# Kernel tuning notes

Hardware: AMD Instinct MI355X
Metric: run time of the kernel (lower is better)

Reference implementation:

```python
import jax, jax.numpy as jnp
import numpy as np
from jax import lax

N = 100000          # nodes in the AST
D = 128             # embedding_dims
C = 8               # max arity (complete 8-ary tree)
NTYPES = 131        # len(NODE_TYPES)


def setup_inputs() -> dict:
    key = jax.random.key(0)
    k_t, k_e, k_ih, k_hh = jax.random.split(key, 4)

    # --- build complete 8-ary tree structure (numpy, static) ---
    idx = np.arange(1, N)
    par = (idx - 1) // C
    slot = (idx - 1) % C
    children = np.full((N, C), N, dtype=np.int32)   # pad with sentinel N
    children[par, slot] = idx
    num_children = np.bincount(par, minlength=N).astype(np.int32)
    # depth of node i in complete C-ary tree: level d starts at (C^d-1)/(C-1)
    starts = np.array([(C ** d - 1) // (C - 1) for d in range(12)], dtype=np.int64)
    depth = np.searchsorted(starts, np.arange(N), side='right') - 1
    L = int(depth.max()) + 1
    M = int(np.bincount(depth).max())
    level_nodes = np.full((L, M), N, dtype=np.int32)  # deepest level first
    for d in range(L):
        nd = np.nonzero(depth == d)[0].astype(np.int32)
        level_nodes[L - 1 - d, : len(nd)] = nd

    # --- parameters (xavier-ish embedding, small LSTM weights, torch bias init) ---
    emb_table = jax.random.normal(k_e, (NTYPES, D), jnp.float32) * (2.0 / (NTYPES + D)) ** 0.5
    W_ih = jax.random.normal(k_ih, (4 * D, D), jnp.float32) * (2.0 / (5 * D)) ** 0.5
    W_hh = jax.random.normal(k_hh, (4 * D, D), jnp.float32) * (2.0 / (5 * D)) ** 0.5
    b_ih = jnp.zeros((4 * D,), jnp.float32)
    b_hh = jnp.ones((4 * D,), jnp.float32)
    node_types = jax.random.randint(k_t, (N,), 0, NTYPES, dtype=jnp.int32)
    return {
        'emb_table': emb_table, 'W_ih': W_ih, 'W_hh': W_hh,
        'b_ih': b_ih, 'b_hh': b_hh,
        'node_types': node_types,
        'children': jnp.asarray(children),
        'num_children': jnp.asarray(num_children),
        'level_nodes': jnp.asarray(level_nodes),
    }


def _forward(emb_table, W_ih, W_hh, b_ih, b_hh, node_types, children, num_children, level_nodes):
    M = level_nodes.shape[1]
    T = C + 1  # sequence length = parent emb + up to C child results

    def level_step(results, nodes):
        # nodes: [M] node ids for this depth level (sentinel N = padding)
        emb = emb_table[node_types[nodes]]            # [M, D] (OOB gather clips; masked below)
        nc = num_children[nodes]                      # [M]
        cres = results[children[nodes]]               # [M, C, D]; sentinel -> zero row N
        seq = jnp.concatenate([emb[:, None, :], cres], axis=1)  # [M, T, D]

        def cell(carry, xt):
            h, c = carry
            x, t = xt
            gates = x @ W_ih.T + b_ih + h @ W_hh.T + b_hh      # [M, 4D]
            i, f, g, o = jnp.split(gates, 4, axis=-1)
            i = jax.nn.sigmoid(i); f = jax.nn.sigmoid(f)
            g = jnp.tanh(g); o = jax.nn.sigmoid(o)
            c_new = f * c + i * g
            h_new = o * jnp.tanh(c_new)
            valid = (t <= nc)[:, None]                         # steps 0..nc are real
            return (jnp.where(valid, h_new, h), jnp.where(valid, c_new, c)), None

        h0 = jnp.zeros((M, emb_table.shape[1]), emb_table.dtype)
        (h, _), _ = lax.scan(cell, (h0, h0), (seq.transpose(1, 0, 2), jnp.arange(T)))
        out = jnp.where((nc == 0)[:, None], emb, h)   # leaves: raw embedding, no LSTM
        results = results.at[nodes].set(out)
        results = results.at[N].set(0.0)              # keep sentinel row zero
        return results, None

    results0 = jnp.zeros((N + 1, emb_table.shape[1]), emb_table.dtype)
    results, _ = lax.scan(level_step, results0, level_nodes)  # deepest -> root
    return results[0]  # root (Module node) encoding, shape [D]


def reference(emb_table, W_ih, W_hh, b_ih, b_hh, node_types, children, num_children, level_nodes):
    return _forward(emb_table, W_ih, W_hh, b_ih, b_hh,
                    node_types, children, num_children, level_nodes)
```

## Files before the change

### kernel.cpp

```cpp
#include <hip/hip_runtime.h>


#define D 128
#define NTOT 100000
#define NINT 12500
#define NTYPES 131

typedef _Float16 f16x8 __attribute__((ext_vector_type(8)));
typedef _Float16 f16x4 __attribute__((ext_vector_type(4)));
typedef float    f32x4 __attribute__((ext_vector_type(4)));

__device__ __forceinline__ float fsig(float x) {
    return __builtin_amdgcn_rcpf(1.f + __expf(-x));
}
__device__ __forceinline__ float ftanh(float x) {
    return 1.f - 2.f * __builtin_amdgcn_rcpf(__expf(2.f * x) + 1.f);
}

template<int DPT> struct XVT;
template<> struct XVT<8> { using T = f16x8; };
template<> struct XVT<4> { using T = f16x4; };

__global__ void prep(const float* __restrict__ W_ih, const float* __restrict__ W_hh,
                     const float* __restrict__ b_ih, const float* __restrict__ b_hh,
                     const float* __restrict__ emb,
                     _Float16* __restrict__ wfrag, float4* __restrict__ bias4,
                     _Float16* __restrict__ embH)
{
    int t = blockIdx.x * blockDim.x + threadIdx.x;
    if (t < 8 * 4 * 8 * 64) {
        int l  = t & 63;
        int kk = (t >> 6) & 7;
        int ct = (t >> 9) & 3;
        int w  = (t >> 11) & 7;
        int k0 = (kk & 3) * 32 + ((l >> 4) * 8);
        int c  = ct * 128 + w * 16 + (l & 15);
        const float* src = (kk < 4) ? (W_ih + (size_t)c * D + k0)
                                    : (W_hh + (size_t)c * D + k0);
        f16x8 v;
#pragma unroll
        for (int j = 0; j < 8; ++j) v[j] = (_Float16)src[j];
        *(f16x8*)(wfrag + (size_t)t * 8) = v;
    }
    if (t < D) {
        bias4[t] = make_float4(b_ih[t      ] + b_hh[t      ],
                               b_ih[t + 128] + b_hh[t + 128],
                               b_ih[t + 256] + b_hh[t + 256],
                               b_ih[t + 384] + b_hh[t + 384]);
    }
    if (t < NTYPES * D / 8) {
        f16x8 v;
#pragma unroll
        for (int j = 0; j < 8; ++j) v[j] = (_Float16)emb[t * 8 + j];
        *(f16x8*)(embH + (size_t)t * 8) = v;
    }
}

template<int RT, bool FUSE_ROOT>
__global__ __launch_bounds__(512) void lstm_level(
    int start, int count,
    const _Float16* __restrict__ embH, const int* __restrict__ node_types,
    const int* __restrict__ children,
    const _Float16* __restrict__ wfrag, const float4* __restrict__ bias4,
    _Float16* __restrict__ resultsH, float* __restrict__ out)
{
    constexpr int NR  = 16 * RT;
    constexpr int TPR = 512 / NR;
    constexpr int DPT = 128 / TPR;
    using xvec = typename XVT<DPT>::T;

    __shared__ __align__(16) _Float16 Xh[2][NR][264];
    __shared__ int chid_s[NR][8];
    __shared__ int chty_s[NR][8];
    __shared__ __align__(16) _Float16 Hstash[8][128];

    const int t  = threadIdx.x;
    const int w  = t >> 6;
    const int l  = t & 63;
    const int n0 = start + (int)blockIdx.x * NR;
    const int B  = min(NR, start + count - n0);

    const int row  = t / TPR;
    const int di   = (t % TPR) * DPT;
    const int dcol = w * 16 + (l & 15);

    if (t < NR * 8) {
        int rr = t >> 3, slot = t & 7;
        int ch = children[(size_t)(n0 + rr) * 8 + slot];
        chid_s[rr][slot] = ch;
        chty_s[rr][slot] = (ch >= NINT && ch < NTOT) ? node_types[ch] : 0;
    }

    f16x8 bf[4][8];
#pragma unroll
    for (int ct = 0; ct < 4; ++ct)
#pragma unroll
        for (int kk = 0; kk < 8; ++kk)
            bf[ct][kk] = *(const f16x8*)(wfrag + ((size_t)(((w * 4 + ct) * 8 + kk) * 64 + l)) * 8);
    const float4 bb = bias4[dcol];

    __syncthreads();

    auto issue_gather = [&](int s) -> xvec {
        const _Float16* src;
        if (s == 0) {
            src = embH + (size_t)node_types[n0 + row] * D + di;
        } else {
            int ch = chid_s[row][s - 1];
            if (ch >= NTOT) return (xvec)(_Float16)0.f;
            src = (ch < NINT) ? (resultsH + (size_t)ch * D + di)
                              : (embH + (size_t)chty_s[row][s - 1] * D + di);
        }
        return *(const xvec*)src;
    };

    *(xvec*)&Xh[0][row][di]       = issue_gather(0);
    *(xvec*)&Xh[0][row][128 + di] = (xvec)(_Float16)0.f;
    xvec xA = issue_gather(1);
    xvec xB = issue_gather(2);

    float cr[RT][4], hr[RT][4];
#pragma unroll
    for (int rt = 0; rt < RT; ++rt)
#pragma unroll
        for (int r = 0; r < 4; ++r) { cr[rt][r] = 0.f; hr[rt][r] = 0.f; }

    f32x4 acc[RT][4];
    auto mfma_phase = [&](int b) {
#pragma unroll
        for (int rt = 0; rt < RT; ++rt)
#pragma unroll
            for (int ct = 0; ct < 4; ++ct) acc[rt][ct] = (f32x4){0.f, 0.f, 0.f, 0.f};
#pragma unroll
        for (int kk = 0; kk < 8; ++kk) {
#pragma unroll
            for (int rt = 0; rt < RT; ++rt) {
                f16x8 a = *(const f16x8*)&Xh[b][rt * 16 + (l & 15)][kk * 32 + ((l >> 4) * 8)];
#pragma unroll
                for (int ct = 0; ct < 4; ++ct)
                    acc[rt][ct] = __builtin_amdgcn_mfma_f32_16x16x32_f16(a, bf[ct][kk], acc[rt][ct], 0, 0, 0);
            }
        }
    };
    auto cell_phase = [&](int s, int b, bool always) {
#pragma unroll
        for (int rt = 0; rt < RT; ++rt)
#pragma unroll
            for (int r = 0; r < 4; ++r) {
                const int r2 = rt * 16 + ((l >> 4) * 4) + r;
                const bool upd = always || (s == 0) || (chid_s[r2][s - 1] < NTOT);
                if (upd) {
                    float iv = fsig (acc[rt][0][r] + bb.x);
                    float fv = fsig (acc[rt][1][r] + bb.y);
                    float gv = ftanh(acc[rt][2][r] + bb.z);
                    float ov = fsig (acc[rt][3][r] + bb.w);
                    float cn = fv * cr[rt][r] + iv * gv;
                    cr[rt][r] = cn;
                    hr[rt][r] = ov * ftanh(cn);
                }
                if (s < 8) Xh[b ^ 1][r2][128 + dcol] = (_Float16)hr[rt][r];
            }
    };

    __syncthreads();

    for (int s = 0; s < 9; ++s) {
        const int b = s & 1;
        mfma_phase(b);
        if (s < 8) {
            *(xvec*)&Xh[b ^ 1][row][di] = xA;
            xA = xB;
            if (s <= 5) xB = issue_gather(s + 3);
        }
        cell_phase(s, b, false);
        __syncthreads();
    }

#pragma unroll
    for (int rt = 0; rt < RT; ++rt)
#pragma unroll
        for (int r = 0; r < 4; ++r) {
            const int r2 = rt * 16 + ((l >> 4) * 4) + r;
            if (r2 < B) {
                resultsH[(size_t)(n0 + r2) * D + dcol] = (_Float16)hr[rt][r];
                if (FUSE_ROOT && r2 < 8) Hstash[r2][dcol] = (_Float16)hr[rt][r];
            }
        }

    if constexpr (FUSE_ROOT) {
        __syncthreads();
        *(xvec*)&Xh[0][row][di]       = *(const xvec*)(embH + (size_t)node_types[0] * D + di);
        *(xvec*)&Xh[0][row][128 + di] = (xvec)(_Float16)0.f;
#pragma unroll
        for (int rt = 0; rt < RT; ++rt)
#pragma unroll
            for (int r = 0; r < 4; ++r) { cr[rt][r] = 0.f; hr[rt][r] = 0.f; }
        __syncthreads();

        for (int s = 0; s < 9; ++s) {
            const int b = s & 1;
            mfma_phase(b);
            if (s < 8)
                *(xvec*)&Xh[b ^ 1][row][di] = *(const xvec*)&Hstash[s][di];
            cell_phase(s, b, true);
            __syncthreads();
        }
        if ((l >> 4) == 0) out[dcol] = hr[0][0];
    }
}

extern "C" void kernel_launch(void* const* d_in, const int* in_sizes, int n_in,
                              void* d_out, int out_size, void* d_ws, size_t ws_size,
                              hipStream_t stream)
{
    const float* emb        = (const float*)d_in[0];
    const float* W_ih       = (const float*)d_in[1];
    const float* W_hh       = (const float*)d_in[2];
    const float* b_ih       = (const float*)d_in[3];
    const float* b_hh       = (const float*)d_in[4];
    const int*   node_types = (const int*)d_in[5];
    const int*   children   = (const int*)d_in[6];

    float* out = (float*)d_out;

    char*      ws       = (char*)d_ws;
    _Float16*  resultsH = (_Float16*)ws;
    size_t     off      = ((size_t)NINT * D * 2 + 255) & ~(size_t)255;
    _Float16*  wfrag    = (_Float16*)(ws + off);
    float4*    bias4    = (float4*)(ws + off + 262144);
    _Float16*  embH     = (_Float16*)(ws + off + 262144 + 2048);

    prep<<<66, 256, 0, stream>>>(W_ih, W_hh, b_ih, b_hh, emb, wfrag, bias4, embH);

    lstm_level<2,false><<<245, 512, 0, stream>>>(4681, 7819, embH, node_types, children,
                                                 wfrag, bias4, resultsH, out);
    lstm_level<1,false><<<256, 512, 0, stream>>>(585, 4096, embH, node_types, children,
                                                 wfrag, bias4, resultsH, out);
    lstm_level<1,false><<<32, 512, 0, stream>>>(73, 512, embH, node_types, children,
                                                wfrag, bias4, resultsH, out);
    lstm_level<1,false><<<4, 512, 0, stream>>>(9, 64, embH, node_types, children,
                                               wfrag, bias4, resultsH, out);
    lstm_level<1,true><<<1, 512, 0, stream>>>(1, 8, embH, node_types, children,
                                              wfrag, bias4, resultsH, out);
}
```

Measured before the change: 106.2 us.

## Fuse prep and all tree levels into one persistent kernel with grid barriers

Replaces the prep kernel and the five per-level launches with a single persistent kernel of 256 blocks that synchronise through atomic-counter grid barriers in global memory. Every level now uses 32-row tiles, so level 2 runs on 128 blocks instead of 256 and the top two levels run serially in block 0. This removes launch gaps and each block reloads its weight fragments only once, but it assumes all 256 blocks are co-resident and it adds spin-wait barrier latency plus less parallelism for the smaller levels.

```diff
diff --git a/kernel.cpp b/kernel.cpp
--- a/kernel.cpp
+++ b/kernel.cpp
@@ -5,9 +5,9 @@
 #define NTOT 100000
 #define NINT 12500
 #define NTYPES 131
+#define NB 256
 
 typedef _Float16 f16x8 __attribute__((ext_vector_type(8)));
-typedef _Float16 f16x4 __attribute__((ext_vector_type(4)));
 typedef float    f32x4 __attribute__((ext_vector_type(4)));
 
 __device__ __forceinline__ float fsig(float x) {
@@ -17,79 +17,79 @@
     return 1.f - 2.f * __builtin_amdgcn_rcpf(__expf(2.f * x) + 1.f);
 }
 
-template<int DPT> struct XVT;
-template<> struct XVT<8> { using T = f16x8; };
-template<> struct XVT<4> { using T = f16x4; };
-
-__global__ void prep(const float* __restrict__ W_ih, const float* __restrict__ W_hh,
-                     const float* __restrict__ b_ih, const float* __restrict__ b_hh,
-                     const float* __restrict__ emb,
-                     _Float16* __restrict__ wfrag, float4* __restrict__ bias4,
-                     _Float16* __restrict__ embH)
+__global__ void bar_init(unsigned* __restrict__ bar) {
+    if (threadIdx.x < 16) bar[threadIdx.x] = 0u;
+}
+
+__global__ __launch_bounds__(512) void tree_lstm(
+    const float* __restrict__ W_ih, const float* __restrict__ W_hh,
+    const float* __restrict__ b_ih, const float* __restrict__ b_hh,
+    const float* __restrict__ emb, const int* __restrict__ node_types,
+    const int* __restrict__ children,
+    _Float16* __restrict__ resultsH, _Float16* __restrict__ wfrag,
+    float4* __restrict__ bias4, _Float16* __restrict__ embH,
+    unsigned* __restrict__ bar, float* __restrict__ out)
 {
-    int t = blockIdx.x * blockDim.x + threadIdx.x;
-    if (t < 8 * 4 * 8 * 64) {
-        int l  = t & 63;
-        int kk = (t >> 6) & 7;
-        int ct = (t >> 9) & 3;
-        int w  = (t >> 11) & 7;
-        int k0 = (kk & 3) * 32 + ((l >> 4) * 8);
-        int c  = ct * 128 + w * 16 + (l & 15);
-        const float* src = (kk < 4) ? (W_ih + (size_t)c * D + k0)
-                                    : (W_hh + (size_t)c * D + k0);
-        f16x8 v;
-#pragma unroll
-        for (int j = 0; j < 8; ++j) v[j] = (_Float16)src[j];
-        *(f16x8*)(wfrag + (size_t)t * 8) = v;
+    __shared__ __align__(16) _Float16 Xh[2][32][264];
+    __shared__ int chid_s[32][8];
+    __shared__ int chty_s[32][8];
+    __shared__ __align__(16) _Float16 Hstash[8][128];
+
+    const int t   = threadIdx.x;
+    const int w   = t >> 6;
+    const int l   = t & 63;
+    const int bid = blockIdx.x;
+    const int row = t >> 4;
+    const int di  = (t & 15) * 8;
+    const int dcol = w * 16 + (l & 15);
+
+    unsigned* cnt  = bar;
+    unsigned* flag = bar + 8;
+
+    auto gbar = [&](int slot) {
+        __syncthreads();
+        if (t == 0) {
+            __threadfence();
+            unsigned old = __hip_atomic_fetch_add(&cnt[slot], 1u,
+                                __ATOMIC_ACQ_REL, __HIP_MEMORY_SCOPE_AGENT);
+            if (old == NB - 1) {
+                __hip_atomic_store(&flag[slot], 1u,
+                                   __ATOMIC_RELEASE, __HIP_MEMORY_SCOPE_AGENT);
+            } else {
+                while (__hip_atomic_load(&flag[slot],
+                           __ATOMIC_ACQUIRE, __HIP_MEMORY_SCOPE_AGENT) == 0u)
+                    __builtin_amdgcn_s_sleep(2);
+            }
+        }
+        __syncthreads();
+    };
+
+    {
+        const int tg = bid * 512 + t;
+        if (tg < 8 * 4 * 8 * 64) {
+            int ll = tg & 63, kk = (tg >> 6) & 7, ct = (tg >> 9) & 3, ww = (tg >> 11) & 7;
+            int k0 = (kk & 3) * 32 + ((ll >> 4) * 8);
+            int c  = ct * 128 + ww * 16 + (ll & 15);
+            const float* src = (kk < 4) ? (W_ih + (size_t)c * D + k0)
+                                        : (W_hh + (size_t)c * D + k0);
+            f16x8 v;
+#pragma unroll
+            for (int j = 0; j < 8; ++j) v[j] = (_Float16)src[j];
+            *(f16x8*)(wfrag + (size_t)tg * 8) = v;
+        }
+        if (tg < D)
+            bias4[tg] = make_float4(b_ih[tg      ] + b_hh[tg      ],
+                                    b_ih[tg + 128] + b_hh[tg + 128],
+                                    b_ih[tg + 256] + b_hh[tg + 256],
+                                    b_ih[tg + 384] + b_hh[tg + 384]);
+        if (tg < NTYPES * D / 8) {
+            f16x8 v;
+#pragma unroll
+            for (int j = 0; j < 8; ++j) v[j] = (_Float16)emb[tg * 8 + j];
+            *(f16x8*)(embH + (size_t)tg * 8) = v;
+        }
     }
-    if (t < D) {
-        bias4[t] = make_float4(b_ih[t      ] + b_hh[t      ],
-                               b_ih[t + 128] + b_hh[t + 128],
-                               b_ih[t + 256] + b_hh[t + 256],
-                               b_ih[t + 384] + b_hh[t + 384]);
-    }
-    if (t < NTYPES * D / 8) {
-        f16x8 v;
-#pragma unroll
-        for (int j = 0; j < 8; ++j) v[j] = (_Float16)emb[t * 8 + j];
-        *(f16x8*)(embH + (size_t)t * 8) = v;
-    }
-}
-
-template<int RT, bool FUSE_ROOT>
-__global__ __launch_bounds__(512) void lstm_level(
-    int start, int count,
-    const _Float16* __restrict__ embH, const int* __restrict__ node_types,
-    const int* __restrict__ children,
-    const _Float16* __restrict__ wfrag, const float4* __restrict__ bias4,
-    _Float16* __restrict__ resultsH, float* __restrict__ out)
-{
-    constexpr int NR  = 16 * RT;
-    constexpr int TPR = 512 / NR;
-    constexpr int DPT = 128 / TPR;
-    using xvec = typename XVT<DPT>::T;
-
-    __shared__ __align__(16) _Float16 Xh[2][NR][264];
-    __shared__ int chid_s[NR][8];
-    __shared__ int chty_s[NR][8];
-    __shared__ __align__(16) _Float16 Hstash[8][128];
-
-    const int t  = threadIdx.x;
-    const int w  = t >> 6;
-    const int l  = t & 63;
-    const int n0 = start + (int)blockIdx.x * NR;
-    const int B  = min(NR, start + count - n0);
-
-    const int row  = t / TPR;
-    const int di   = (t % TPR) * DPT;
-    const int dcol = w * 16 + (l & 15);
-
-    if (t < NR * 8) {
-        int rr = t >> 3, slot = t & 7;
-        int ch = children[(size_t)(n0 + rr) * 8 + slot];
-        chid_s[rr][slot] = ch;
-        chty_s[rr][slot] = (ch >= NINT && ch < NTOT) ? node_types[ch] : 0;
-    }
+    gbar(0);
 
     f16x8 bf[4][8];
 #pragma unroll
@@ -99,42 +99,18 @@
             bf[ct][kk] = *(const f16x8*)(wfrag + ((size_t)(((w * 4 + ct) * 8 + kk) * 64 + l)) * 8);
     const float4 bb = bias4[dcol];
 
-    __syncthreads();
-
-    auto issue_gather = [&](int s) -> xvec {
-        const _Float16* src;
-        if (s == 0) {
-            src = embH + (size_t)node_types[n0 + row] * D + di;
-        } else {
-            int ch = chid_s[row][s - 1];
-            if (ch >= NTOT) return (xvec)(_Float16)0.f;
-            src = (ch < NINT) ? (resultsH + (size_t)ch * D + di)
-                              : (embH + (size_t)chty_s[row][s - 1] * D + di);
-        }
-        return *(const xvec*)src;
-    };
-
-    *(xvec*)&Xh[0][row][di]       = issue_gather(0);
-    *(xvec*)&Xh[0][row][128 + di] = (xvec)(_Float16)0.f;
-    xvec xA = issue_gather(1);
-    xvec xB = issue_gather(2);
-
-    float cr[RT][4], hr[RT][4];
-#pragma unroll
-    for (int rt = 0; rt < RT; ++rt)
-#pragma unroll
-        for (int r = 0; r < 4; ++r) { cr[rt][r] = 0.f; hr[rt][r] = 0.f; }
-
-    f32x4 acc[RT][4];
+    float cr[2][4], hr[2][4];
+    f32x4 acc[2][4];
+
     auto mfma_phase = [&](int b) {
 #pragma unroll
-        for (int rt = 0; rt < RT; ++rt)
+        for (int rt = 0; rt < 2; ++rt)
 #pragma unroll
             for (int ct = 0; ct < 4; ++ct) acc[rt][ct] = (f32x4){0.f, 0.f, 0.f, 0.f};
 #pragma unroll
         for (int kk = 0; kk < 8; ++kk) {
 #pragma unroll
-            for (int rt = 0; rt < RT; ++rt) {
+            for (int rt = 0; rt < 2; ++rt) {
                 f16x8 a = *(const f16x8*)&Xh[b][rt * 16 + (l & 15)][kk * 32 + ((l >> 4) * 8)];
 #pragma unroll
                 for (int ct = 0; ct < 4; ++ct)
@@ -144,7 +120,7 @@
     };
     auto cell_phase = [&](int s, int b, bool always) {
 #pragma unroll
-        for (int rt = 0; rt < RT; ++rt)
+        for (int rt = 0; rt < 2; ++rt)
 #pragma unroll
             for (int r = 0; r < 4; ++r) {
                 const int r2 = rt * 16 + ((l >> 4) * 4) + r;
@@ -162,37 +138,82 @@
             }
     };
 
-    __syncthreads();
-
-    for (int s = 0; s < 9; ++s) {
-        const int b = s & 1;
-        mfma_phase(b);
-        if (s < 8) {
-            *(xvec*)&Xh[b ^ 1][row][di] = xA;
-            xA = xB;
-            if (s <= 5) xB = issue_gather(s + 3);
-        }
-        cell_phase(s, b, false);
-        __syncthreads();
-    }
-
-#pragma unroll
-    for (int rt = 0; rt < RT; ++rt)
-#pragma unroll
-        for (int r = 0; r < 4; ++r) {
-            const int r2 = rt * 16 + ((l >> 4) * 4) + r;
-            if (r2 < B) {
-                resultsH[(size_t)(n0 + r2) * D + dcol] = (_Float16)hr[rt][r];
-                if (FUSE_ROOT && r2 < 8) Hstash[r2][dcol] = (_Float16)hr[rt][r];
-            }
-        }
-
-    if constexpr (FUSE_ROOT) {
-        __syncthreads();
-        *(xvec*)&Xh[0][row][di]       = *(const xvec*)(embH + (size_t)node_types[0] * D + di);
-        *(xvec*)&Xh[0][row][128 + di] = (xvec)(_Float16)0.f;
-#pragma unroll
-        for (int rt = 0; rt < RT; ++rt)
+    auto do_tile = [&](int start, int count, int tile, bool stash) {
+        const int n0 = start + tile * 32;
+        const int B  = min(32, start + count - n0);
+
+        if (t < 256) {
+            int rr = t >> 3, slot = t & 7;
+            int ch = children[(size_t)(n0 + rr) * 8 + slot];
+            chid_s[rr][slot] = ch;
+            chty_s[rr][slot] = (ch >= NINT && ch < NTOT) ? node_types[ch] : 0;
+        }
+        __syncthreads();
+
+        auto issue_gather = [&](int s) -> f16x8 {
+            const _Float16* src;
+            if (s == 0) {
+                src = embH + (size_t)node_types[n0 + row] * D + di;
+            } else {
+                int ch = chid_s[row][s - 1];
+                if (ch >= NTOT) return (f16x8)(_Float16)0.f;
+                src = (ch < NINT) ? (resultsH + (size_t)ch * D + di)
+                                  : (embH + (size_t)chty_s[row][s - 1] * D + di);
+            }
+            return *(const f16x8*)src;
+        };
+
+        *(f16x8*)&Xh[0][row][di]       = issue_gather(0);
+        *(f16x8*)&Xh[0][row][128 + di] = (f16x8)(_Float16)0.f;
+        f16x8 xA = issue_gather(1);
+        f16x8 xB = issue_gather(2);
+#pragma unroll
+        for (int rt = 0; rt < 2; ++rt)
+#pragma unroll
+            for (int r = 0; r < 4; ++r) { cr[rt][r] = 0.f; hr[rt][r] = 0.f; }
+        __syncthreads();
+
+        for (int s = 0; s < 9; ++s) {
+            const int b = s & 1;
+            mfma_phase(b);
+            if (s < 8) {
+                *(f16x8*)&Xh[b ^ 1][row][di] = xA;
+                xA = xB;
+                if (s <= 5) xB = issue_gather(s + 3);
+            }
+            cell_phase(s, b, false);
+            __syncthreads();
+        }
+
+#pragma unroll
+        for (int rt = 0; rt < 2; ++rt)
+#pragma unroll
+            for (int r = 0; r < 4; ++r) {
+                const int r2 = rt * 16 + ((l >> 4) * 4) + r;
+                if (r2 < B) {
+                    resultsH[(size_t)(n0 + r2) * D + dcol] = (_Float16)hr[rt][r];
+                    if (stash && r2 < 8) Hstash[r2][dcol] = (_Float16)hr[rt][r];
+                }
+            }
+    };
+
+    if (bid < 245) do_tile(4681, 7819, bid, false);
+    gbar(1);
+    if (bid < 128) do_tile(585, 4096, bid, false);
+    gbar(2);
+    if (bid < 16)  do_tile(73, 512, bid, false);
+    gbar(3);
+
+    if (bid == 0) {
+        do_tile(9, 64, 0, false);
+        do_tile(9, 64, 1, false);
+        do_tile(1, 8, 0, true);
+
+        __syncthreads();
+        *(f16x8*)&Xh[0][row][di]       = *(const f16x8*)(embH + (size_t)node_types[0] * D + di);
+        *(f16x8*)&Xh[0][row][128 + di] = (f16x8)(_Float16)0.f;
+#pragma unroll
+        for (int rt = 0; rt < 2; ++rt)
 #pragma unroll
             for (int r = 0; r < 4; ++r) { cr[rt][r] = 0.f; hr[rt][r] = 0.f; }
         __syncthreads();
@@ -201,7 +222,7 @@
             const int b = s & 1;
             mfma_phase(b);
             if (s < 8)
-                *(xvec*)&Xh[b ^ 1][row][di] = *(const xvec*)&Hstash[s][di];
+                *(f16x8*)&Xh[b ^ 1][row][di] = *(const f16x8*)&Hstash[s][di];
             cell_phase(s, b, true);
             __syncthreads();
         }
@@ -229,17 +250,9 @@
     _Float16*  wfrag    = (_Float16*)(ws + off);
     float4*    bias4    = (float4*)(ws + off + 262144);
     _Float16*  embH     = (_Float16*)(ws + off + 262144 + 2048);
-
-    prep<<<66, 256, 0, stream>>>(W_ih, W_hh, b_ih, b_hh, emb, wfrag, bias4, embH);
-
-    lstm_level<2,false><<<245, 512, 0, stream>>>(4681, 7819, embH, node_types, children,
-                                                 wfrag, bias4, resultsH, out);
-    lstm_level<1,false><<<256, 512, 0, stream>>>(585, 4096, embH, node_types, children,
-                                                 wfrag, bias4, resultsH, out);
-    lstm_level<1,false><<<32, 512, 0, stream>>>(73, 512, embH, node_types, children,
-                                                wfrag, bias4, resultsH, out);
-    lstm_level<1,false><<<4, 512, 0, stream>>>(9, 64, embH, node_types, children,
-                                               wfrag, bias4, resultsH, out);
-    lstm_level<1,true><<<1, 512, 0, stream>>>(1, 8, embH, node_types, children,
-                                              wfrag, bias4, resultsH, out);
-}
+    unsigned*  barp     = (unsigned*)(ws + off + 262144 + 2048 + 33536);
+
+    bar_init<<<1, 64, 0, stream>>>(barp);
+    tree_lstm<<<NB, 512, 0, stream>>>(W_ih, W_hh, b_ih, b_hh, emb, node_types, children,
+                                      resultsH, wfrag, bias4, embH, barp, out);
+}
```

Result: slower. 269.3 us (+153.5%).
